# Performance work log

Hardware: AMD Instinct MI355X
Metric: run time of the kernel (lower is better)

The kernel has to match this reference:

```python
import jax, jax.numpy as jnp
import numpy as np

B = 64            # number of graphs
NPG = 64          # nodes per graph (static; lengths are all equal here)
N = B * NPG       # total nodes = sum(lengths)
LT = 128          # max text tokens per node
LL = 32           # max labels per node
VOCAB = 50000
TOTAL_NUM = 100000
D = 256           # embedding_text == embedding_label == hidden_dimension
OUT = 1024


def setup_inputs() -> dict:
    key = jax.random.key(0)
    ks = jax.random.split(key, 12)
    return {
        "text_ids": jax.random.randint(ks[0], (N, LT), 0, VOCAB),
        "label_ids": jax.random.randint(ks[1], (N, LL), 0, TOTAL_NUM),
        "text_len": jax.random.randint(ks[2], (N,), 1, LT + 1),
        "label_len": jax.random.randint(ks[3], (N,), 1, LL + 1),
        "word_emb": jax.random.normal(ks[4], (VOCAB, D), jnp.float32) * 0.02,
        "label_emb": jax.random.normal(ks[5], (TOTAL_NUM, D), jnp.float32) * 0.02,
        "Wg_text": jax.random.normal(ks[6], (D, D), jnp.float32) * (1.0 / np.sqrt(D)),
        "Wg_label": jax.random.normal(ks[7], (D, D), jnp.float32) * (1.0 / np.sqrt(D)),
        "w_adap": jax.random.normal(ks[8], (2,), jnp.float32),
        "W1": jax.random.normal(ks[9], (D, D), jnp.float32) * (1.0 / np.sqrt(D)),
        "b1": jnp.zeros((D,), jnp.float32),
        "Wout": jax.random.normal(ks[10], (D, OUT), jnp.float32) * (1.0 / np.sqrt(D)),
        "bout": jnp.zeros((OUT,), jnp.float32),
    }


def _ragged_bag(table, ids, lens, mean):
    # gather rows then masked sum over the ragged axis (EmbeddingBag-style)
    L = ids.shape[1]
    mask = (jnp.arange(L)[None, :] < lens[:, None]).astype(table.dtype)  # [N, L]
    emb = table[ids]                                                     # [N, L, D]
    out = jnp.einsum("nld,nl->nd", emb, mask)
    if mean:
        out = out / lens[:, None].astype(table.dtype)
    return out


def reference(text_ids, label_ids, text_len, label_len, word_emb, label_emb,
              Wg_text, Wg_label, w_adap, W1, b1, Wout, bout):
    # fetchFeature: per-node ragged mean of word embeddings, ragged sum of label embeddings
    text_out = _ragged_bag(word_emb, text_ids, text_len, mean=True)    # [N, D]
    label_out = _ragged_bag(label_emb, label_ids, label_len, mean=False)  # [N, D]

    # weighted_GCN surrogate: per-type linear projection + relu, then per-graph mean readout
    h_t = jax.nn.relu(text_out @ Wg_text)   # [N, D]
    h_l = jax.nn.relu(label_out @ Wg_label)  # [N, D]
    seg = jnp.repeat(jnp.arange(B), NPG)     # graph id per node
    r_t = jax.ops.segment_sum(h_t, seg, num_segments=B) / NPG  # [B, D]
    r_l = jax.ops.segment_sum(h_l, seg, num_segments=B) / NPG  # [B, D]

    # adap: Linear(2,1,bias=False) over stacked (text,label), then MLLinear fusion
    fused = jnp.stack([r_t, r_l], axis=-1) @ w_adap  # [B, D]
    h = jax.nn.relu(fused @ W1 + b1)
    return h @ Wout + bout  # [B, OUT]
```

## Files before the change

### kernel.cpp

```cpp
#include <hip/hip_runtime.h>

#define NN      4096
#define BG      64
#define NPG_    64
#define LT_     128
#define LL_     32
#define D_      256
#define OUT_    1024
#define VOCAB_  50000

typedef __attribute__((ext_vector_type(8))) short bf16x8;
typedef __attribute__((ext_vector_type(4))) float f32x4;

__device__ __forceinline__ unsigned short f2bf_rne(float f) {
    union { float f; unsigned u; } a; a.f = f;
    const unsigned r = a.u + 0x7FFFu + ((a.u >> 16) & 1u);
    return (unsigned short)(r >> 16);
}
__device__ __forceinline__ float bf2f(unsigned short h) {
    union { unsigned u; float f; } a; a.u = ((unsigned)h) << 16;
    return a.f;
}
__device__ __forceinline__ void split_bf16(float v, unsigned short& hi, unsigned short& lo) {
    union { float f; unsigned u; } a; a.f = v;
    const unsigned hu = (a.u + 0x8000u) & 0xFFFF0000u;
    union { unsigned u; float f; } h; h.u = hu;
    const float r = v - h.f;
    union { float f; unsigned u; } b; b.f = r;
    hi = (unsigned short)(hu >> 16);
    lo = (unsigned short)(((b.u + 0x8000u) & 0xFFFF0000u) >> 16);
}

__global__ __launch_bounds__(256) void prep_kernel(
    const float* __restrict__ word_emb,
    const float* __restrict__ Wg_text,
    const float* __restrict__ Wg_label,
    const int convBlocks,
    unsigned short* __restrict__ wtab,
    unsigned short* __restrict__ Wpk)
{
    const int tid = threadIdx.x;
    if (blockIdx.x < convBlocks) {
        const int total4 = VOCAB_ * D_ / 4;
        const int stride = convBlocks * 256;
        for (int i = blockIdx.x * 256 + tid; i < total4; i += stride) {
            const float4 v = *reinterpret_cast<const float4*>(word_emb + (size_t)i * 4);
            ushort4 o;
            o.x = f2bf_rne(v.x); o.y = f2bf_rne(v.y);
            o.z = f2bf_rne(v.z); o.w = f2bf_rne(v.w);
            *reinterpret_cast<ushort4*>(wtab + (size_t)i * 4) = o;
        }
        return;
    }
    const int b   = blockIdx.x - convBlocks;
    const int mat = b >> 7;
    const int nt  = (b >> 3) & 15;
    const int ks  = b & 7;
    const float* __restrict__ W = mat ? Wg_label : Wg_text;
    #pragma unroll
    for (int r = 0; r < 2; ++r) {
        const int idx = tid + 256 * r;
        const int kl  = idx >> 4;
        const int c16 = idx & 15;
        const int k   = ks * 32 + kl;
        const float v = W[(size_t)k * D_ + nt * 16 + c16];
        unsigned short h, l;
        split_bf16(v, h, l);
        const int lane = c16 + 16 * ((kl >> 3) & 3);
        const int e    = kl & 7;
        const size_t pb = (((size_t)nt * 8 + ks) * 4 + mat * 2) * 512 + lane * 8 + e;
        Wpk[pb]       = h;
        Wpk[pb + 512] = l;
    }
}

template<bool BF16TAB>
__global__ __launch_bounds__(256) void gather_kernel(
    const int*   __restrict__ text_ids,
    const int*   __restrict__ label_ids,
    const int*   __restrict__ text_len,
    const int*   __restrict__ label_len,
    const float* __restrict__ word_emb,
    const unsigned short* __restrict__ wtab,
    const float* __restrict__ label_emb,
    unsigned short* __restrict__ xb_t,
    unsigned short* __restrict__ xb_l)
{
    __shared__ int   sIds[LT_ + LL_];
    __shared__ float red[8][D_];

    const int n    = blockIdx.x;
    const int tid  = threadIdx.x;
    const int wave = tid >> 6;
    const int lane = tid & 63;

    if (tid < LT_)               sIds[tid] = text_ids [(size_t)n * LT_ + tid];
    else if (tid < LT_ + LL_)    sIds[tid] = label_ids[(size_t)n * LL_ + (tid - LT_)];
    const int lt = text_len[n];
    const int ll = label_len[n];
    __syncthreads();

    float ta[8];
    float4 aT4 = make_float4(0.f, 0.f, 0.f, 0.f);
    if (BF16TAB) {
        #pragma unroll
        for (int j = 0; j < 8; ++j) ta[j] = 0.f;
        const int h  = lane >> 5;
        const int cg = lane & 31;
        const int s  = wave * 2 + h;
        const unsigned short* __restrict__ bp = wtab + cg * 8;
        #pragma unroll 4
        for (int l = s; l < lt; l += 8) {
            const bf16x8 v = *reinterpret_cast<const bf16x8*>(bp + (size_t)sIds[l] * D_);
            #pragma unroll
            for (int j = 0; j < 8; ++j) ta[j] += bf2f((unsigned short)v[j]);
        }
    } else {
        const float* __restrict__ bp = word_emb + (size_t)lane * 4;
        #pragma unroll 8
        for (int l = wave; l < lt; l += 4) {
            const float4 v = *reinterpret_cast<const float4*>(bp + (size_t)sIds[l] * D_);
            aT4.x += v.x; aT4.y += v.y; aT4.z += v.z; aT4.w += v.w;
        }
    }

    float4 aL = make_float4(0.f, 0.f, 0.f, 0.f);
    {
        const float* __restrict__ bp = label_emb + (size_t)lane * 4;
        #pragma unroll 8
        for (int l = wave; l < ll; l += 4) {
            const float4 v = *reinterpret_cast<const float4*>(bp + (size_t)sIds[LT_ + l] * D_);
            aL.x += v.x; aL.y += v.y; aL.z += v.z; aL.w += v.w;
        }
    }

    if (BF16TAB) {
        const int h = lane >> 5, cg = lane & 31, s = wave * 2 + h;
        *reinterpret_cast<float4*>(&red[s][cg * 8])     = make_float4(ta[0], ta[1], ta[2], ta[3]);
        *reinterpret_cast<float4*>(&red[s][cg * 8 + 4]) = make_float4(ta[4], ta[5], ta[6], ta[7]);
    } else {
        *reinterpret_cast<float4*>(&red[wave][lane * 4]) = aT4;
    }
    __syncthreads();
    float t;
    if (BF16TAB)
        t = ((red[0][tid] + red[1][tid]) + (red[2][tid] + red[3][tid]))
          + ((red[4][tid] + red[5][tid]) + (red[6][tid] + red[7][tid]));
    else
        t = (red[0][tid] + red[1][tid]) + (red[2][tid] + red[3][tid]);
    t /= (float)lt;
    const size_t o = (size_t)n * D_ + tid;
    xb_t[o] = f2bf_rne(t);
    __syncthreads();

    *reinterpret_cast<float4*>(&red[wave][lane * 4]) = aL;
    __syncthreads();
    const float lv = (red[0][tid] + red[1][tid]) + (red[2][tid] + red[3][tid]);
    xb_l[o] = f2bf_rne(lv);
}

__global__ __launch_bounds__(256, 4) void proj_kernel(
    const unsigned short* __restrict__ xb_t,
    const unsigned short* __restrict__ xb_l,
    const unsigned short* __restrict__ Wpk,
    const float* __restrict__ w_adap,
    float*       __restrict__ h_comb)
{
    __shared__ __align__(16) short ldsX[2][16 * D_];

    const int tid   = threadIdx.x;
    const int wave  = tid >> 6;
    const int lane  = tid & 63;
    const int ntile = blockIdx.x >> 2;
    const int cq    = blockIdx.x & 3;
    const int base  = ntile * 16;

    #pragma unroll
    for (int r = 0; r < 2; ++r) {
        const int idx = tid + 256 * r;
        const int nd  = idx >> 5, ch = idx & 31;
        const size_t g = (size_t)(base + nd) * D_ + ch * 8;
        const int d = nd * D_ + ((ch ^ (nd & 7)) * 8);
        *reinterpret_cast<int4*>(&ldsX[0][d]) = *reinterpret_cast<const int4*>(&xb_t[g]);
        *reinterpret_cast<int4*>(&ldsX[1][d]) = *reinterpret_cast<const int4*>(&xb_l[g]);
    }
    __syncthreads();

    const int nt  = cq * 4 + wave;
    const int row = lane & 15;
    const int kc  = lane >> 4;
    const unsigned short* __restrict__ WpB = Wpk + ((size_t)nt * 8) * 4 * 512 + lane * 8;

    f32x4 accT = {0.f, 0.f, 0.f, 0.f};
    f32x4 accL = {0.f, 0.f, 0.f, 0.f};

    bf16x8 cA0, cA1, cB0, cB1, cB2, cB3;
    bf16x8 nA0, nA1, nB0, nB1, nB2, nB3;

    {
        const int aidx = row * D_ + ((kc ^ (row & 7)) * 8);
        cA0 = *reinterpret_cast<const bf16x8*>(&ldsX[0][aidx]);
        cA1 = *reinterpret_cast<const bf16x8*>(&ldsX[1][aidx]);
        const unsigned short* p = WpB;
        cB0 = *reinterpret_cast<const bf16x8*>(p);
        cB1 = *reinterpret_cast<const bf16x8*>(p + 512);
        cB2 = *reinterpret_cast<const bf16x8*>(p + 1024);
        cB3 = *reinterpret_cast<const bf16x8*>(p + 1536);
    }

    #pragma unroll
    for (int ks = 0; ks < 8; ++ks) {
        if (ks < 7) {
            const int aidx = row * D_ + ((((ks + 1) * 4 + kc) ^ (row & 7)) * 8);
            nA0 = *reinterpret_cast<const bf16x8*>(&ldsX[0][aidx]);
            nA1 = *reinterpret_cast<const bf16x8*>(&ldsX[1][aidx]);
            const unsigned short* p = WpB + (size_t)(ks + 1) * 2048;
            nB0 = *reinterpret_cast<const bf16x8*>(p);
            nB1 = *reinterpret_cast<const bf16x8*>(p + 512);
            nB2 = *reinterpret_cast<const bf16x8*>(p + 1024);
            nB3 = *reinterpret_cast<const bf16x8*>(p + 1536);
        }

        accT = __builtin_amdgcn_mfma_f32_16x16x32_bf16(cA0, cB0, accT, 0, 0, 0);
        accT = __builtin_amdgcn_mfma_f32_16x16x32_bf16(cA0, cB1, accT, 0, 0, 0);
        accL = __builtin_amdgcn_mfma_f32_16x16x32_bf16(cA1, cB2, accL, 0, 0, 0);
        accL = __builtin_amdgcn_mfma_f32_16x16x32_bf16(cA1, cB3, accL, 0, 0, 0);

        cA0 = nA0; cA1 = nA1;
        cB0 = nB0; cB1 = nB1; cB2 = nB2; cB3 = nB3;
    }

    const float w0r = w_adap[0] * (1.0f / (float)NPG_);
    const float w1r = w_adap[1] * (1.0f / (float)NPG_);
    #pragma unroll
    for (int r = 0; r < 4; ++r) {
        const int node = base + kc * 4 + r;
        const int col  = nt * 16 + row;
        const float ht = accT[r] > 0.f ? accT[r] : 0.f;
        const float hl = accL[r] > 0.f ? accL[r] : 0.f;
        h_comb[(size_t)node * D_ + col] = w0r * ht + w1r * hl;
    }
}

__global__ __launch_bounds__(256) void graph_kernel(
    const float* __restrict__ h_comb,
    const float* __restrict__ W1,
    const float* __restrict__ b1,
    const float* __restrict__ Wout,
    const float* __restrict__ bout,
    float*       __restrict__ out)
{
    __shared__ float fused[D_];
    __shared__ float hrow[D_];

    const int bx   = blockIdx.x;
    const int b    = bx >> 2;
    const int part = bx & 3;
    const int tid  = threadIdx.x;

    float acc = 0.f;
    const float* __restrict__ basep = h_comb + (size_t)b * NPG_ * D_ + tid;
    #pragma unroll 8
    for (int n = 0; n < NPG_; ++n) acc += basep[(size_t)n * D_];
    fused[tid] = acc;
    __syncthreads();

    {
        float s0 = 0.f, s1 = 0.f, s2 = 0.f, s3 = 0.f;
        const float* __restrict__ wp = W1 + tid;
        for (int d = 0; d < D_; d += 4) {
            s0 = fmaf(fused[d + 0], wp[(size_t)(d + 0) * D_], s0);
            s1 = fmaf(fused[d + 1], wp[(size_t)(d + 1) * D_], s1);
            s2 = fmaf(fused[d + 2], wp[(size_t)(d + 2) * D_], s2);
            s3 = fmaf(fused[d + 3], wp[(size_t)(d + 3) * D_], s3);
        }
        const float a1 = b1[tid] + ((s0 + s1) + (s2 + s3));
        hrow[tid] = a1 > 0.f ? a1 : 0.f;
    }
    __syncthreads();

    const int j = part * 256 + tid;
    {
        float s0 = 0.f, s1 = 0.f, s2 = 0.f, s3 = 0.f;
        const float* __restrict__ wp = Wout + j;
        for (int d = 0; d < D_; d += 4) {
            s0 = fmaf(hrow[d + 0], wp[(size_t)(d + 0) * OUT_], s0);
            s1 = fmaf(hrow[d + 1], wp[(size_t)(d + 1) * OUT_], s1);
            s2 = fmaf(hrow[d + 2], wp[(size_t)(d + 2) * OUT_], s2);
            s3 = fmaf(hrow[d + 3], wp[(size_t)(d + 3) * OUT_], s3);
        }
        out[(size_t)b * OUT_ + j] = bout[j] + ((s0 + s1) + (s2 + s3));
    }
}

extern "C" void kernel_launch(void* const* d_in, const int* in_sizes, int n_in,
                              void* d_out, int out_size, void* d_ws, size_t ws_size,
                              hipStream_t stream) {
    const int*   text_ids  = (const int*)  d_in[0];
    const int*   label_ids = (const int*)  d_in[1];
    const int*   text_len  = (const int*)  d_in[2];
    const int*   label_len = (const int*)  d_in[3];
    const float* word_emb  = (const float*)d_in[4];
    const float* label_emb = (const float*)d_in[5];
    const float* Wg_text   = (const float*)d_in[6];
    const float* Wg_label  = (const float*)d_in[7];
    const float* w_adap    = (const float*)d_in[8];
    const float* W1        = (const float*)d_in[9];
    const float* b1        = (const float*)d_in[10];
    const float* Wout      = (const float*)d_in[11];
    const float* bout      = (const float*)d_in[12];

    char* ws = (char*)d_ws;
    float*          h_comb = (float*)ws;
    unsigned short* xb_t   = (unsigned short*)(ws + (4 << 20));
    unsigned short* xb_l   = (unsigned short*)(ws + (6 << 20));
    unsigned short* Wpk    = (unsigned short*)(ws + (8 << 20));
    unsigned short* wtab   = (unsigned short*)(ws + (9 << 20));
    float*          out    = (float*)d_out;

    const size_t need = (size_t)(9 << 20) + (size_t)VOCAB_ * D_ * 2;
    const bool useBf16 = ws_size >= need;
    const int convBlocks = useBf16 ? 2048 : 0;

    prep_kernel<<<convBlocks + 256, 256, 0, stream>>>(
        word_emb, Wg_text, Wg_label, convBlocks, wtab, Wpk);

    if (useBf16) {
        gather_kernel<true><<<NN, 256, 0, stream>>>(
            text_ids, label_ids, text_len, label_len,
            word_emb, wtab, label_emb, xb_t, xb_l);
    } else {
        gather_kernel<false><<<NN, 256, 0, stream>>>(
            text_ids, label_ids, text_len, label_len,
            word_emb, wtab, label_emb, xb_t, xb_l);
    }

    proj_kernel<<<NN / 16 * 4, 256, 0, stream>>>(
        xb_t, xb_l, Wpk, w_adap, h_comb);

    graph_kernel<<<BG * 4, 256, 0, stream>>>(
        h_comb, W1, b1, Wout, bout, out);
}
```

Before: 75.41 us.

## Move label-bag gather into prep kernel to overlap with table conversion

The label embedding bag gather moves out of the text gather kernel and into the prep kernel as extra blocks, so it runs alongside the word-table bf16 conversion and weight packing. The text gather kernel now only handles text tokens, which shortens its per-block critical path and LDS use. This trades a larger prep launch for better overlap of independent work and a lighter text gather. It may hurt if the extra label blocks compete for bandwidth with the table conversion.

```diff
diff --git a/kernel.cpp b/kernel.cpp
--- a/kernel.cpp
+++ b/kernel.cpp
@@ -31,15 +31,20 @@
     lo = (unsigned short)(((b.u + 0x8000u) & 0xFFFF0000u) >> 16);
 }
 
-__global__ __launch_bounds__(256) void prep_kernel(
+__global__ __launch_bounds__(256) void prep_label_kernel(
     const float* __restrict__ word_emb,
     const float* __restrict__ Wg_text,
     const float* __restrict__ Wg_label,
     const int convBlocks,
+    const int*   __restrict__ label_ids,
+    const int*   __restrict__ label_len,
+    const float* __restrict__ label_emb,
     unsigned short* __restrict__ wtab,
-    unsigned short* __restrict__ Wpk)
+    unsigned short* __restrict__ Wpk,
+    unsigned short* __restrict__ xb_l)
 {
     const int tid = threadIdx.x;
+
     if (blockIdx.x < convBlocks) {
         const int total4 = VOCAB_ * D_ / 4;
         const int stride = convBlocks * 256;
@@ -52,41 +57,65 @@
         }
         return;
     }
-    const int b   = blockIdx.x - convBlocks;
-    const int mat = b >> 7;
-    const int nt  = (b >> 3) & 15;
-    const int ks  = b & 7;
-    const float* __restrict__ W = mat ? Wg_label : Wg_text;
-    #pragma unroll
-    for (int r = 0; r < 2; ++r) {
-        const int idx = tid + 256 * r;
-        const int kl  = idx >> 4;
-        const int c16 = idx & 15;
-        const int k   = ks * 32 + kl;
-        const float v = W[(size_t)k * D_ + nt * 16 + c16];
-        unsigned short h, l;
-        split_bf16(v, h, l);
-        const int lane = c16 + 16 * ((kl >> 3) & 3);
-        const int e    = kl & 7;
-        const size_t pb = (((size_t)nt * 8 + ks) * 4 + mat * 2) * 512 + lane * 8 + e;
-        Wpk[pb]       = h;
-        Wpk[pb + 512] = l;
-    }
+    if (blockIdx.x < convBlocks + 256) {
+        const int b   = blockIdx.x - convBlocks;
+        const int mat = b >> 7;
+        const int nt  = (b >> 3) & 15;
+        const int ks  = b & 7;
+        const float* __restrict__ W = mat ? Wg_label : Wg_text;
+        #pragma unroll
+        for (int r = 0; r < 2; ++r) {
+            const int idx = tid + 256 * r;
+            const int kl  = idx >> 4;
+            const int c16 = idx & 15;
+            const int k   = ks * 32 + kl;
+            const float v = W[(size_t)k * D_ + nt * 16 + c16];
+            unsigned short h, l;
+            split_bf16(v, h, l);
+            const int lane = c16 + 16 * ((kl >> 3) & 3);
+            const int e    = kl & 7;
+            const size_t pb = (((size_t)nt * 8 + ks) * 4 + mat * 2) * 512 + lane * 8 + e;
+            Wpk[pb]       = h;
+            Wpk[pb + 512] = l;
+        }
+        return;
+    }
+
+    __shared__ int   sIds[LL_];
+    __shared__ float red[4][D_];
+
+    const int n    = blockIdx.x - convBlocks - 256;
+    const int wave = tid >> 6;
+    const int lane = tid & 63;
+
+    if (tid < LL_) sIds[tid] = label_ids[(size_t)n * LL_ + tid];
+    const int ll = label_len[n];
+    __syncthreads();
+
+    float4 aL = make_float4(0.f, 0.f, 0.f, 0.f);
+    {
+        const float* __restrict__ bp = label_emb + (size_t)lane * 4;
+        #pragma unroll 8
+        for (int l = wave; l < ll; l += 4) {
+            const float4 v = *reinterpret_cast<const float4*>(bp + (size_t)sIds[l] * D_);
+            aL.x += v.x; aL.y += v.y; aL.z += v.z; aL.w += v.w;
+        }
+    }
+    *reinterpret_cast<float4*>(&red[wave][lane * 4]) = aL;
+    __syncthreads();
+    const float lv = (red[0][tid] + red[1][tid]) + (red[2][tid] + red[3][tid]);
+    xb_l[(size_t)n * D_ + tid] = f2bf_rne(lv);
 }
 
 template<bool BF16TAB>
-__global__ __launch_bounds__(256) void gather_kernel(
+__global__ __launch_bounds__(256) void textg_kernel(
     const int*   __restrict__ text_ids,
-    const int*   __restrict__ label_ids,
     const int*   __restrict__ text_len,
-    const int*   __restrict__ label_len,
     const float* __restrict__ word_emb,
     const unsigned short* __restrict__ wtab,
-    const float* __restrict__ label_emb,
-    unsigned short* __restrict__ xb_t,
-    unsigned short* __restrict__ xb_l)
+    unsigned short* __restrict__ xb_t)
 {
-    __shared__ int   sIds[LT_ + LL_];
+    __shared__ int   sIds[LT_];
     __shared__ float red[8][D_];
 
     const int n    = blockIdx.x;
@@ -94,15 +123,13 @@
     const int wave = tid >> 6;
     const int lane = tid & 63;
 
-    if (tid < LT_)               sIds[tid] = text_ids [(size_t)n * LT_ + tid];
-    else if (tid < LT_ + LL_)    sIds[tid] = label_ids[(size_t)n * LL_ + (tid - LT_)];
+    if (tid < LT_) sIds[tid] = text_ids[(size_t)n * LT_ + tid];
     const int lt = text_len[n];
-    const int ll = label_len[n];
-    __syncthreads();
-
-    float ta[8];
-    float4 aT4 = make_float4(0.f, 0.f, 0.f, 0.f);
+    __syncthreads();
+
+    float t;
     if (BF16TAB) {
+        float ta[8];
         #pragma unroll
         for (int j = 0; j < 8; ++j) ta[j] = 0.f;
         const int h  = lane >> 5;
@@ -115,48 +142,25 @@
             #pragma unroll
             for (int j = 0; j < 8; ++j) ta[j] += bf2f((unsigned short)v[j]);
         }
+        *reinterpret_cast<float4*>(&red[s][cg * 8])     = make_float4(ta[0], ta[1], ta[2], ta[3]);
+        *reinterpret_cast<float4*>(&red[s][cg * 8 + 4]) = make_float4(ta[4], ta[5], ta[6], ta[7]);
+        __syncthreads();
+        t = ((red[0][tid] + red[1][tid]) + (red[2][tid] + red[3][tid]))
+          + ((red[4][tid] + red[5][tid]) + (red[6][tid] + red[7][tid]));
     } else {
+        float4 a4 = make_float4(0.f, 0.f, 0.f, 0.f);
         const float* __restrict__ bp = word_emb + (size_t)lane * 4;
         #pragma unroll 8
         for (int l = wave; l < lt; l += 4) {
             const float4 v = *reinterpret_cast<const float4*>(bp + (size_t)sIds[l] * D_);
-            aT4.x += v.x; aT4.y += v.y; aT4.z += v.z; aT4.w += v.w;
-        }
-    }
-
-    float4 aL = make_float4(0.f, 0.f, 0.f, 0.f);
-    {
-        const float* __restrict__ bp = label_emb + (size_t)lane * 4;
-        #pragma unroll 8
-        for (int l = wave; l < ll; l += 4) {
-            const float4 v = *reinterpret_cast<const float4*>(bp + (size_t)sIds[LT_ + l] * D_);
-            aL.x += v.x; aL.y += v.y; aL.z += v.z; aL.w += v.w;
-        }
-    }
-
-    if (BF16TAB) {
-        const int h = lane >> 5, cg = lane & 31, s = wave * 2 + h;
-        *reinterpret_cast<float4*>(&red[s][cg * 8])     = make_float4(ta[0], ta[1], ta[2], ta[3]);
-        *reinterpret_cast<float4*>(&red[s][cg * 8 + 4]) = make_float4(ta[4], ta[5], ta[6], ta[7]);
-    } else {
-        *reinterpret_cast<float4*>(&red[wave][lane * 4]) = aT4;
-    }
-    __syncthreads();
-    float t;
-    if (BF16TAB)
-        t = ((red[0][tid] + red[1][tid]) + (red[2][tid] + red[3][tid]))
-          + ((red[4][tid] + red[5][tid]) + (red[6][tid] + red[7][tid]));
-    else
+            a4.x += v.x; a4.y += v.y; a4.z += v.z; a4.w += v.w;
+        }
+        *reinterpret_cast<float4*>(&red[wave][lane * 4]) = a4;
+        __syncthreads();
         t = (red[0][tid] + red[1][tid]) + (red[2][tid] + red[3][tid]);
+    }
     t /= (float)lt;
-    const size_t o = (size_t)n * D_ + tid;
-    xb_t[o] = f2bf_rne(t);
-    __syncthreads();
-
-    *reinterpret_cast<float4*>(&red[wave][lane * 4]) = aL;
-    __syncthreads();
-    const float lv = (red[0][tid] + red[1][tid]) + (red[2][tid] + red[3][tid]);
-    xb_l[o] = f2bf_rne(lv);
+    xb_t[(size_t)n * D_ + tid] = f2bf_rne(t);
 }
 
 __global__ __launch_bounds__(256, 4) void proj_kernel(
@@ -322,17 +326,17 @@
     const bool useBf16 = ws_size >= need;
     const int convBlocks = useBf16 ? 2048 : 0;
 
-    prep_kernel<<<convBlocks + 256, 256, 0, stream>>>(
-        word_emb, Wg_text, Wg_label, convBlocks, wtab, Wpk);
+    prep_label_kernel<<<convBlocks + 256 + NN, 256, 0, stream>>>(
+        word_emb, Wg_text, Wg_label, convBlocks,
+        label_ids, label_len, label_emb,
+        wtab, Wpk, xb_l);
 
     if (useBf16) {
-        gather_kernel<true><<<NN, 256, 0, stream>>>(
-            text_ids, label_ids, text_len, label_len,
-            word_emb, wtab, label_emb, xb_t, xb_l);
+        textg_kernel<true><<<NN, 256, 0, stream>>>(
+            text_ids, text_len, word_emb, wtab, xb_t);
     } else {
-        gather_kernel<false><<<NN, 256, 0, stream>>>(
-            text_ids, label_ids, text_len, label_len,
-            word_emb, wtab, label_emb, xb_t, xb_l);
+        textg_kernel<false><<<NN, 256, 0, stream>>>(
+            text_ids, text_len, word_emb, wtab, xb_t);
     }
 
     proj_kernel<<<NN / 16 * 4, 256, 0, stream>>>(
```

After: 74.22 us. Within noise of the previous version (-1.6%).
